# Performance work log

Hardware: AMD Instinct MI355X
Metric: run time of the kernel (lower is better)

## Reference

```python
import jax, jax.numpy as jnp
import numpy as np
import math

B, S, H = 512, 100, 1024
A, N = 128, 8
TAU = 1.0


def make_pe(seq_len, hidden):
    # PositionalEncoding buffer: pe[s, 0::2]=sin(pos*div), pe[s,1::2]=cos(pos*div)
    pos = jnp.arange(seq_len, dtype=jnp.float32)[:, None]          # [S,1]
    div = jnp.exp(jnp.arange(0, hidden, 2, dtype=jnp.float32) * (-math.log(10000.0) / hidden))
    pe = jnp.zeros((seq_len, hidden), dtype=jnp.float32)
    pe = pe.at[:, 0::2].set(jnp.sin(pos * div))
    pe = pe.at[:, 1::2].set(jnp.cos(pos * div))
    return pe                                                      # [S,H]


def setup_inputs() -> dict:
    key = jax.random.key(0)
    kx, kq, kk, kg = jax.random.split(key, 4)
    x = jax.random.normal(kx, (B, S, H), dtype=jnp.float32)
    # torch Linear weight layout: [out_features, in_features]
    Wq = jax.random.normal(kq, (A * N, H), dtype=jnp.float32) * (1.0 / math.sqrt(H))
    Wk = jax.random.normal(kk, (A * N, H), dtype=jnp.float32) * (1.0 / math.sqrt(H))
    # pre-sampled standard Gumbel noise (deterministic reference)
    u = jax.random.uniform(kg, (B * N, S), dtype=jnp.float32, minval=1e-6, maxval=1.0 - 1e-6)
    gumbel = -jnp.log(-jnp.log(u))
    return {"x": x, "Wq": Wq, "Wk": Wk, "gumbel": gumbel}


def reference(x, Wq, Wk, gumbel):
    b, s, h = x.shape
    pos_emb = x + make_pe(s, h)[None]                              # [B,S,H]
    Q = (pos_emb @ Wq.T).reshape(b, s, N, A).transpose(0, 2, 1, 3)  # [B,N,S,A]
    K = (pos_emb @ Wk.T).reshape(b, s, N, A).transpose(0, 2, 1, 3)  # [B,N,S,A]
    # original: sum_t (Q . K_t) / sqrt(H) / S  ==  Q . (sum_t K_t) / (sqrt(H)*S)
    Ksum = K.sum(axis=2)                                           # [B,N,A]
    logits = jnp.einsum('bnsa,bna->bns', Q, Ksum) / (math.sqrt(h) * s)
    y = (logits.reshape(b * N, s) + gumbel) / TAU
    soft = jax.nn.softmax(y, axis=-1)
    hard = jax.nn.one_hot(jnp.argmax(y, axis=-1), s, dtype=soft.dtype)
    # straight-through (forward value == hard one-hot)
    alphas = (hard - jax.lax.stop_gradient(soft) + soft).reshape(b, N, s)
    out = jnp.einsum('bns,bsh->bnh', alphas, x)                    # gather selected timesteps
    return out
```

## Files before the change

### kernel.cpp

```cpp
#include <hip/hip_runtime.h>
#include <float.h>
#include <math.h>

#define Bc 512
#define Sc 100
#define Hc 1024
#define Ac 128
#define Nc 8
#define AS_ST 68
#define BS_ST 132

__global__ __launch_bounds__(256) void pe_kernel(float* __restrict__ pe){
  int s = blockIdx.x;
  int t = threadIdx.x;
  const float fac = (float)(-9.210340371976184 / 1024.0);
  for(int i = t; i < Hc/2; i += 256){
    float div = expf((float)(2*i) * fac);
    float a = (float)s * div;
    pe[s*Hc + 2*i]     = sinf(a);
    pe[s*Hc + 2*i + 1] = cosf(a);
  }
}

__global__ __launch_bounds__(256) void pesum_kernel(const float* __restrict__ pe, float* __restrict__ pesum){
  int h = blockIdx.x*256 + threadIdx.x;
  float acc = 0.f;
  for(int s = 0; s < Sc; ++s) acc += pe[s*Hc + h];
  pesum[h] = acc;
}

__global__ __launch_bounds__(256) void xsum_kernel(const float* __restrict__ x, const float* __restrict__ pesum,
                                                   float* __restrict__ xsp){
  int b = blockIdx.x;
  int q = blockIdx.y;
  int t = threadIdx.x;
  const float4* xr = (const float4*)(x + (size_t)b*Sc*Hc);
  float4 acc;
  if(q == 0) acc = ((const float4*)pesum)[t];
  else       acc = make_float4(0.f,0.f,0.f,0.f);
  int s0 = q*25;
  #pragma unroll 5
  for(int s = s0; s < s0+25; ++s){
    float4 v = xr[s*(Hc/4) + t];
    acc.x += v.x; acc.y += v.y; acc.z += v.z; acc.w += v.w;
  }
  ((float4*)(xsp + ((size_t)b*4 + q)*Hc))[t] = acc;
}

__global__ __launch_bounds__(256) void xsred_kernel(const float* __restrict__ xsp, float* __restrict__ xs){
  int b = blockIdx.x, t = threadIdx.x;
  const float4* p = (const float4*)(xsp + (size_t)b*4*Hc);
  float4 a = p[t], b1 = p[256+t], c = p[512+t], d = p[768+t];
  a.x += b1.x + c.x + d.x;
  a.y += b1.y + c.y + d.y;
  a.z += b1.z + c.z + d.z;
  a.w += b1.w + c.w + d.w;
  ((float4*)(xs + (size_t)b*Hc))[t] = a;
}

__global__ __launch_bounds__(256) void ksum_gemm2(const float* __restrict__ xs, const float* __restrict__ Wk,
                                                  float* __restrict__ Ksum8){
  __shared__ float As[32*AS_ST];
  __shared__ float Bs[32*BS_ST];
  const int t = threadIdx.x;
  const int j0 = blockIdx.x*128, b0 = blockIdx.y*64, ks = blockIdx.z;
  const int ty = t>>4, tx = t&15;
  float acc[4][8];
  #pragma unroll
  for(int i = 0; i < 4; ++i)
    #pragma unroll
    for(int j = 0; j < 8; ++j) acc[i][j] = 0.f;

  const int kb = ks*128;
  float4 af[2], bf[4], afn[2], bfn[4];
  #pragma unroll
  for(int i = 0; i < 2; ++i){
    int id = t + i*256; int m = id>>3, q = id&7;
    af[i] = *(const float4*)(xs + ((size_t)(b0+m)<<10) + kb + q*4);
  }
  #pragma unroll
  for(int i = 0; i < 4; ++i){
    int id = t + i*256; int r = id>>3, c = id&7;
    bf[i] = *(const float4*)(Wk + ((size_t)(j0+r)<<10) + kb + c*4);
  }

  for(int c0 = 0; c0 < 4; ++c0){
    __syncthreads();
    #pragma unroll
    for(int i = 0; i < 2; ++i){
      int id = t + i*256; int m = id>>3, q = id&7;
      As[(q*4+0)*AS_ST + m] = af[i].x;
      As[(q*4+1)*AS_ST + m] = af[i].y;
      As[(q*4+2)*AS_ST + m] = af[i].z;
      As[(q*4+3)*AS_ST + m] = af[i].w;
    }
    #pragma unroll
    for(int i = 0; i < 4; ++i){
      int id = t + i*256; int r = id>>3, c = id&7;
      Bs[(c*4+0)*BS_ST + r] = bf[i].x;
      Bs[(c*4+1)*BS_ST + r] = bf[i].y;
      Bs[(c*4+2)*BS_ST + r] = bf[i].z;
      Bs[(c*4+3)*BS_ST + r] = bf[i].w;
    }
    if(c0 < 3){
      int k0 = kb + (c0+1)*32;
      #pragma unroll
      for(int i = 0; i < 2; ++i){
        int id = t + i*256; int m = id>>3, q = id&7;
        afn[i] = *(const float4*)(xs + ((size_t)(b0+m)<<10) + k0 + q*4);
      }
      #pragma unroll
      for(int i = 0; i < 4; ++i){
        int id = t + i*256; int r = id>>3, c = id&7;
        bfn[i] = *(const float4*)(Wk + ((size_t)(j0+r)<<10) + k0 + c*4);
      }
    }
    __syncthreads();
    #pragma unroll 8
    for(int kk = 0; kk < 32; ++kk){
      float4 a4 = *(const float4*)&As[kk*AS_ST + ty*4];
      float4 bu = *(const float4*)&Bs[kk*BS_ST + tx*4];
      float4 bv = *(const float4*)&Bs[kk*BS_ST + 64 + tx*4];
      float a[4] = {a4.x, a4.y, a4.z, a4.w};
      float bb[8] = {bu.x,bu.y,bu.z,bu.w, bv.x,bv.y,bv.z,bv.w};
      #pragma unroll
      for(int i = 0; i < 4; ++i)
        #pragma unroll
        for(int j = 0; j < 8; ++j)
          acc[i][j] = fmaf(a[i], bb[j], acc[i][j]);
    }
    af[0]=afn[0]; af[1]=afn[1];
    bf[0]=bfn[0]; bf[1]=bfn[1]; bf[2]=bfn[2]; bf[3]=bfn[3];
  }
  #pragma unroll
  for(int i = 0; i < 4; ++i){
    float* cp = Ksum8 + (((size_t)ks*Bc + b0 + ty*4 + i)<<10) + j0 + tx*4;
    *(float4*)cp        = make_float4(acc[i][0],acc[i][1],acc[i][2],acc[i][3]);
    *(float4*)(cp + 64) = make_float4(acc[i][4],acc[i][5],acc[i][6],acc[i][7]);
  }
}

__global__ __launch_bounds__(256) void ksred8_kernel(const float* __restrict__ Ksum8, float* __restrict__ Ksum){
  int b = blockIdx.x, t = threadIdx.x;
  const float4* p = (const float4*)(Ksum8 + ((size_t)b<<10));
  const size_t sl = (size_t)Bc*Hc/4;
  float4 a = p[t];
  #pragma unroll
  for(int i = 1; i < 8; ++i){
    float4 q = p[i*sl + t];
    a.x += q.x; a.y += q.y; a.z += q.z; a.w += q.w;
  }
  ((float4*)(Ksum + ((size_t)b<<10)))[t] = a;
}

__global__ __launch_bounds__(256) void v_gemm2(const float* __restrict__ Ksum, const float* __restrict__ Wq,
                                               float* __restrict__ v){
  __shared__ float As[32*AS_ST];
  __shared__ float Bs[32*BS_ST];
  const int t = threadIdx.x;
  const int h0 = blockIdx.x*128, b0 = blockIdx.y*64, n = blockIdx.z;
  const int ty = t>>4, tx = t&15;
  float acc[4][8];
  #pragma unroll
  for(int i = 0; i < 4; ++i)
    #pragma unroll
    for(int j = 0; j < 8; ++j) acc[i][j] = 0.f;

  float4 af[2], bf[4], afn[2], bfn[4];
  #pragma unroll
  for(int i = 0; i < 2; ++i){
    int id = t + i*256; int m = id>>3, q = id&7;
    af[i] = *(const float4*)(Ksum + ((size_t)(b0+m)<<10) + n*Ac + q*4);
  }
  #pragma unroll
  for(int i = 0; i < 4; ++i){
    int id = t + i*256; int kk = id>>5, q = id&31;
    bf[i] = *(const float4*)(Wq + ((size_t)(n*Ac + kk)<<10) + h0 + q*4);
  }

  for(int c0 = 0; c0 < 4; ++c0){
    __syncthreads();
    #pragma unroll
    for(int i = 0; i < 2; ++i){
      int id = t + i*256; int m = id>>3, q = id&7;
      As[(q*4+0)*AS_ST + m] = af[i].x;
      As[(q*4+1)*AS_ST + m] = af[i].y;
      As[(q*4+2)*AS_ST + m] = af[i].z;
      As[(q*4+3)*AS_ST + m] = af[i].w;
    }
    #pragma unroll
    for(int i = 0; i < 4; ++i){
      int id = t + i*256; int kk = id>>5, q = id&31;
      *(float4*)&Bs[kk*BS_ST + q*4] = bf[i];
    }
    if(c0 < 3){
      int k0 = (c0+1)*32;
      #pragma unroll
      for(int i = 0; i < 2; ++i){
        int id = t + i*256; int m = id>>3, q = id&7;
        afn[i] = *(const float4*)(Ksum + ((size_t)(b0+m)<<10) + n*Ac + k0 + q*4);
      }
      #pragma unroll
      for(int i = 0; i < 4; ++i){
        int id = t + i*256; int kk = id>>5, q = id&31;
        bfn[i] = *(const float4*)(Wq + ((size_t)(n*Ac + k0 + kk)<<10) + h0 + q*4);
      }
    }
    __syncthreads();
    #pragma unroll 8
    for(int kk = 0; kk < 32; ++kk){
      float4 a4 = *(const float4*)&As[kk*AS_ST + ty*4];
      float4 bu = *(const float4*)&Bs[kk*BS_ST + tx*4];
      float4 bv = *(const float4*)&Bs[kk*BS_ST + 64 + tx*4];
      float a[4] = {a4.x, a4.y, a4.z, a4.w};
      float bb[8] = {bu.x,bu.y,bu.z,bu.w, bv.x,bv.y,bv.z,bv.w};
      #pragma unroll
      for(int i = 0; i < 4; ++i)
        #pragma unroll
        for(int j = 0; j < 8; ++j)
          acc[i][j] = fmaf(a[i], bb[j], acc[i][j]);
    }
    af[0]=afn[0]; af[1]=afn[1];
    bf[0]=bfn[0]; bf[1]=bfn[1]; bf[2]=bfn[2]; bf[3]=bfn[3];
  }
  #pragma unroll
  for(int i = 0; i < 4; ++i){
    float* cp = v + (((size_t)(b0 + ty*4 + i)*Nc + n)<<10) + h0 + tx*4;
    *(float4*)cp        = make_float4(acc[i][0],acc[i][1],acc[i][2],acc[i][3]);
    *(float4*)(cp + 64) = make_float4(acc[i][4],acc[i][5],acc[i][6],acc[i][7]);
  }
}

__global__ __launch_bounds__(1024) void attn_kernel(const float* __restrict__ x, const float* __restrict__ pe,
                                                    const float* __restrict__ v, const float* __restrict__ g,
                                                    float* __restrict__ out){
  __shared__ float4 tile[1600];
  __shared__ float part[8][Nc][104];
  __shared__ int sidx[Nc];
  const int b = blockIdx.x;
  const int t = threadIdx.x;
  const int lane = t & 63;
  const int w  = __builtin_amdgcn_readfirstlane(t >> 6);
  const int kq = w & 7, sh = w >> 3;

  const int r1 = t >> 4, c1 = t & 15;
  const bool has2 = (t < 576);
  const int e2 = t + 1024;
  const int r2 = e2 >> 4, c2 = e2 & 15;

  const float* xb = x + (size_t)b*Sc*Hc;
  const float* vb = v + (size_t)b*Nc*Hc;

  int rw = sh*64 + lane;
  int r  = (rw < Sc) ? rw : (Sc-1);
  const bool valid = (rw < Sc);

  float acc[Nc];
  #pragma unroll
  for(int n = 0; n < Nc; ++n) acc[n] = 0.f;

  float4 xv1 = *(const float4*)(xb + r1*Hc + c1*4);
  float4 pv1 = *(const float4*)(pe + r1*Hc + c1*4);
  float4 xv2 = make_float4(0,0,0,0), pv2 = make_float4(0,0,0,0);
  if(has2){ xv2 = *(const float4*)(xb + r2*Hc + c2*4);
            pv2 = *(const float4*)(pe + r2*Hc + c2*4); }

  for(int kt = 0; kt < 16; ++kt){
    __syncthreads();
    tile[r1*16 + (c1 ^ (r1&7))] = make_float4(xv1.x+pv1.x, xv1.y+pv1.y, xv1.z+pv1.z, xv1.w+pv1.w);
    if(has2)
      tile[r2*16 + (c2 ^ (r2&7))] = make_float4(xv2.x+pv2.x, xv2.y+pv2.y, xv2.z+pv2.z, xv2.w+pv2.w);
    if(kt < 15){
      int ko = (kt+1)*64;
      xv1 = *(const float4*)(xb + r1*Hc + ko + c1*4);
      pv1 = *(const float4*)(pe + r1*Hc + ko + c1*4);
      if(has2){ xv2 = *(const float4*)(xb + r2*Hc + ko + c2*4);
                pv2 = *(const float4*)(pe + r2*Hc + ko + c2*4); }
    }
    __syncthreads();
    #pragma unroll
    for(int j = 0; j < 2; ++j){
      float4 xe = tile[r*16 + ((kq*2 + j) ^ (r&7))];
      const float* vk = vb + kt*64 + kq*8 + j*4;
      #pragma unroll
      for(int n = 0; n < Nc; ++n){
        const float* vn = vk + n*Hc;
        acc[n] = fmaf(xe.x, vn[0], acc[n]);
        acc[n] = fmaf(xe.y, vn[1], acc[n]);
        acc[n] = fmaf(xe.z, vn[2], acc[n]);
        acc[n] = fmaf(xe.w, vn[3], acc[n]);
      }
    }
  }
  if(valid){
    #pragma unroll
    for(int n = 0; n < Nc; ++n) part[kq][n][rw] = acc[n];
  }
  __syncthreads();

  if(w < Nc){
    int n = w, j = lane;
    float best = -FLT_MAX; int bidx = 0;
    #pragma unroll
    for(int i = 0; i < 2; ++i){
      int s2 = j + 64*i;
      if(s2 < Sc){
        float dot = 0.f;
        #pragma unroll
        for(int q = 0; q < 8; ++q) dot += part[q][n][s2];
        float y = dot/3200.0f + g[(size_t)(b*Nc + n)*Sc + s2];
        if(y > best){ best = y; bidx = s2; }
      }
    }
    #pragma unroll
    for(int m = 32; m >= 1; m >>= 1){
      float ob = __shfl_xor(best, m, 64);
      int   oi = __shfl_xor(bidx, m, 64);
      if(ob > best || (ob == best && oi < bidx)){ best = ob; bidx = oi; }
    }
    if(j == 0) sidx[n] = bidx;
  }
  __syncthreads();

  const float4* xb4 = (const float4*)xb;
  float4* ob4 = (float4*)(out + (size_t)b*Nc*Hc);
  #pragma unroll
  for(int i = 0; i < 2; ++i){
    int idx = i*1024 + t;
    int nn = idx >> 8, c = idx & 255;
    ob4[idx] = xb4[sidx[nn]*256 + c];
  }
}

extern "C" void kernel_launch(void* const* d_in, const int* in_sizes, int n_in,
                              void* d_out, int out_size, void* d_ws, size_t ws_size,
                              hipStream_t stream) {
  const float* x  = (const float*)d_in[0];
  const float* Wq = (const float*)d_in[1];
  const float* Wk = (const float*)d_in[2];
  const float* g  = (const float*)d_in[3];
  float* out = (float*)d_out;

  char* ws = (char*)d_ws;
  float* pe    = (float*)(ws);
  float* pesum = (float*)(ws +    409600);
  float* xsp   = (float*)(ws +    413696);
  float* xs    = (float*)(ws +   8802304);
  float* Ksum8 = (float*)(ws +  10899456);
  float* Ksum  = (float*)(ws +  27676672);
  float* v     = (float*)(ws +    413696);

  pe_kernel    <<<100, 256, 0, stream>>>(pe);
  pesum_kernel <<<4,   256, 0, stream>>>(pe, pesum);
  xsum_kernel  <<<dim3(512,4), 256, 0, stream>>>(x, pesum, xsp);
  xsred_kernel <<<512, 256, 0, stream>>>(xsp, xs);
  ksum_gemm2   <<<dim3(8,8,8), 256, 0, stream>>>(xs, Wk, Ksum8);
  ksred8_kernel<<<512, 256, 0, stream>>>(Ksum8, Ksum);
  v_gemm2      <<<dim3(8,8,8), 256, 0, stream>>>(Ksum, Wq, v);
  attn_kernel  <<<512, 1024, 0, stream>>>(x, pe, v, g, out);
}
```

Baseline: 146.2 us.

## Fuse reduction kernels, halve K split-k, and fold partial-sum reduction into v GEMM

```diff
diff --git a/kernel.cpp b/kernel.cpp
--- a/kernel.cpp
+++ b/kernel.cpp
@@ -22,44 +22,39 @@
   }
 }
 
-__global__ __launch_bounds__(256) void pesum_kernel(const float* __restrict__ pe, float* __restrict__ pesum){
-  int h = blockIdx.x*256 + threadIdx.x;
-  float acc = 0.f;
-  for(int s = 0; s < Sc; ++s) acc += pe[s*Hc + h];
-  pesum[h] = acc;
-}
-
-__global__ __launch_bounds__(256) void xsum_kernel(const float* __restrict__ x, const float* __restrict__ pesum,
-                                                   float* __restrict__ xsp){
+__global__ __launch_bounds__(1024) void xsum_fused(const float* __restrict__ x, const float* __restrict__ pe,
+                                                   float* __restrict__ xs){
+  __shared__ float4 part[3][256];
   int b = blockIdx.x;
-  int q = blockIdx.y;
   int t = threadIdx.x;
+  int sg = t >> 8, hc = t & 255;
   const float4* xr = (const float4*)(x + (size_t)b*Sc*Hc);
-  float4 acc;
-  if(q == 0) acc = ((const float4*)pesum)[t];
-  else       acc = make_float4(0.f,0.f,0.f,0.f);
-  int s0 = q*25;
+  const float4* pr = (const float4*)pe;
+  float4 acc = make_float4(0.f,0.f,0.f,0.f);
+  int s0 = sg*25;
   #pragma unroll 5
   for(int s = s0; s < s0+25; ++s){
-    float4 v = xr[s*(Hc/4) + t];
-    acc.x += v.x; acc.y += v.y; acc.z += v.z; acc.w += v.w;
-  }
-  ((float4*)(xsp + ((size_t)b*4 + q)*Hc))[t] = acc;
-}
-
-__global__ __launch_bounds__(256) void xsred_kernel(const float* __restrict__ xsp, float* __restrict__ xs){
-  int b = blockIdx.x, t = threadIdx.x;
-  const float4* p = (const float4*)(xsp + (size_t)b*4*Hc);
-  float4 a = p[t], b1 = p[256+t], c = p[512+t], d = p[768+t];
-  a.x += b1.x + c.x + d.x;
-  a.y += b1.y + c.y + d.y;
-  a.z += b1.z + c.z + d.z;
-  a.w += b1.w + c.w + d.w;
-  ((float4*)(xs + (size_t)b*Hc))[t] = a;
+    float4 v = xr[s*256 + hc];
+    float4 p = pr[s*256 + hc];
+    acc.x += v.x + p.x;
+    acc.y += v.y + p.y;
+    acc.z += v.z + p.z;
+    acc.w += v.w + p.w;
+  }
+  if(sg) part[sg-1][hc] = acc;
+  __syncthreads();
+  if(sg == 0){
+    #pragma unroll
+    for(int i = 0; i < 3; ++i){
+      float4 p = part[i][hc];
+      acc.x += p.x; acc.y += p.y; acc.z += p.z; acc.w += p.w;
+    }
+    ((float4*)(xs + (size_t)b*Hc))[hc] = acc;
+  }
 }
 
 __global__ __launch_bounds__(256) void ksum_gemm2(const float* __restrict__ xs, const float* __restrict__ Wk,
-                                                  float* __restrict__ Ksum8){
+                                                  float* __restrict__ Ksum4){
   __shared__ float As[32*AS_ST];
   __shared__ float Bs[32*BS_ST];
   const int t = threadIdx.x;
@@ -71,7 +66,7 @@
     #pragma unroll
     for(int j = 0; j < 8; ++j) acc[i][j] = 0.f;
 
-  const int kb = ks*128;
+  const int kb = ks*256;
   float4 af[2], bf[4], afn[2], bfn[4];
   #pragma unroll
   for(int i = 0; i < 2; ++i){
@@ -84,7 +79,7 @@
     bf[i] = *(const float4*)(Wk + ((size_t)(j0+r)<<10) + kb + c*4);
   }
 
-  for(int c0 = 0; c0 < 4; ++c0){
+  for(int c0 = 0; c0 < 8; ++c0){
     __syncthreads();
     #pragma unroll
     for(int i = 0; i < 2; ++i){
@@ -102,7 +97,7 @@
       Bs[(c*4+2)*BS_ST + r] = bf[i].z;
       Bs[(c*4+3)*BS_ST + r] = bf[i].w;
     }
-    if(c0 < 3){
+    if(c0 < 7){
       int k0 = kb + (c0+1)*32;
       #pragma unroll
       for(int i = 0; i < 2; ++i){
@@ -134,32 +129,20 @@
   }
   #pragma unroll
   for(int i = 0; i < 4; ++i){
-    float* cp = Ksum8 + (((size_t)ks*Bc + b0 + ty*4 + i)<<10) + j0 + tx*4;
+    float* cp = Ksum4 + (((size_t)ks*Bc + b0 + ty*4 + i)<<10) + j0 + tx*4;
     *(float4*)cp        = make_float4(acc[i][0],acc[i][1],acc[i][2],acc[i][3]);
     *(float4*)(cp + 64) = make_float4(acc[i][4],acc[i][5],acc[i][6],acc[i][7]);
   }
 }
 
-__global__ __launch_bounds__(256) void ksred8_kernel(const float* __restrict__ Ksum8, float* __restrict__ Ksum){
-  int b = blockIdx.x, t = threadIdx.x;
-  const float4* p = (const float4*)(Ksum8 + ((size_t)b<<10));
-  const size_t sl = (size_t)Bc*Hc/4;
-  float4 a = p[t];
-  #pragma unroll
-  for(int i = 1; i < 8; ++i){
-    float4 q = p[i*sl + t];
-    a.x += q.x; a.y += q.y; a.z += q.z; a.w += q.w;
-  }
-  ((float4*)(Ksum + ((size_t)b<<10)))[t] = a;
-}
-
-__global__ __launch_bounds__(256) void v_gemm2(const float* __restrict__ Ksum, const float* __restrict__ Wq,
+__global__ __launch_bounds__(256) void v_gemm2(const float* __restrict__ Ksum4, const float* __restrict__ Wq,
                                                float* __restrict__ v){
   __shared__ float As[32*AS_ST];
   __shared__ float Bs[32*BS_ST];
   const int t = threadIdx.x;
   const int h0 = blockIdx.x*128, b0 = blockIdx.y*64, n = blockIdx.z;
   const int ty = t>>4, tx = t&15;
+  const size_t sl = (size_t)Bc*Hc;
   float acc[4][8];
   #pragma unroll
   for(int i = 0; i < 4; ++i)
@@ -170,7 +153,13 @@
   #pragma unroll
   for(int i = 0; i < 2; ++i){
     int id = t + i*256; int m = id>>3, q = id&7;
-    af[i] = *(const float4*)(Ksum + ((size_t)(b0+m)<<10) + n*Ac + q*4);
+    const float* ap = Ksum4 + ((size_t)(b0+m)<<10) + n*Ac + q*4;
+    float4 a0 = *(const float4*)(ap);
+    float4 a1 = *(const float4*)(ap + sl);
+    float4 a2 = *(const float4*)(ap + 2*sl);
+    float4 a3 = *(const float4*)(ap + 3*sl);
+    af[i] = make_float4(a0.x+a1.x+a2.x+a3.x, a0.y+a1.y+a2.y+a3.y,
+                        a0.z+a1.z+a2.z+a3.z, a0.w+a1.w+a2.w+a3.w);
   }
   #pragma unroll
   for(int i = 0; i < 4; ++i){
@@ -198,7 +187,13 @@
       #pragma unroll
       for(int i = 0; i < 2; ++i){
         int id = t + i*256; int m = id>>3, q = id&7;
-        afn[i] = *(const float4*)(Ksum + ((size_t)(b0+m)<<10) + n*Ac + k0 + q*4);
+        const float* ap = Ksum4 + ((size_t)(b0+m)<<10) + n*Ac + k0 + q*4;
+        float4 a0 = *(const float4*)(ap);
+        float4 a1 = *(const float4*)(ap + sl);
+        float4 a2 = *(const float4*)(ap + 2*sl);
+        float4 a3 = *(const float4*)(ap + 3*sl);
+        afn[i] = make_float4(a0.x+a1.x+a2.x+a3.x, a0.y+a1.y+a2.y+a3.y,
+                             a0.z+a1.z+a2.z+a3.z, a0.w+a1.w+a2.w+a3.w);
       }
       #pragma unroll
       for(int i = 0; i < 4; ++i){
@@ -343,19 +338,13 @@
 
   char* ws = (char*)d_ws;
   float* pe    = (float*)(ws);
-  float* pesum = (float*)(ws +    409600);
-  float* xsp   = (float*)(ws +    413696);
-  float* xs    = (float*)(ws +   8802304);
-  float* Ksum8 = (float*)(ws +  10899456);
-  float* Ksum  = (float*)(ws +  27676672);
-  float* v     = (float*)(ws +    413696);
-
-  pe_kernel    <<<100, 256, 0, stream>>>(pe);
-  pesum_kernel <<<4,   256, 0, stream>>>(pe, pesum);
-  xsum_kernel  <<<dim3(512,4), 256, 0, stream>>>(x, pesum, xsp);
-  xsred_kernel <<<512, 256, 0, stream>>>(xsp, xs);
-  ksum_gemm2   <<<dim3(8,8,8), 256, 0, stream>>>(xs, Wk, Ksum8);
-  ksred8_kernel<<<512, 256, 0, stream>>>(Ksum8, Ksum);
-  v_gemm2      <<<dim3(8,8,8), 256, 0, stream>>>(Ksum, Wq, v);
-  attn_kernel  <<<512, 1024, 0, stream>>>(x, pe, v, g, out);
-}
+  float* xs    = (float*)(ws +    409600);
+  float* Ksum4 = (float*)(ws +   2506752);
+  float* v     = (float*)(ws +  10895360);
+
+  pe_kernel  <<<100, 256, 0, stream>>>(pe);
+  xsum_fused <<<512, 1024, 0, stream>>>(x, pe, xs);
+  ksum_gemm2 <<<dim3(8,8,4), 256, 0, stream>>>(xs, Wk, Ksum4);
+  v_gemm2    <<<dim3(8,8,8), 256, 0, stream>>>(Ksum4, Wq, v);
+  attn_kernel<<<512, 1024, 0, stream>>>(x, pe, v, g, out);
+}
```

Result: no change. 149.0 us (+1.9%).
